# Optimization experiments

Hardware: AMD Instinct MI355X
Metric: run time of the kernel (lower is better)

The kernel has to match this reference:

```python
import jax, jax.numpy as jnp
import numpy as np

N_NODES = 100000
N_EDGES = 1600000
H_IN = 128
H_OUT = 128
ELU_ALPHA = 0.1


def setup_inputs() -> dict:
    key = jax.random.key(0)
    k = jax.random.split(key, 6)
    x = jax.random.normal(k[0], (N_NODES, H_IN), dtype=jnp.float32)
    edge_index = jax.random.randint(k[1], (2, N_EDGES), 0, N_NODES, dtype=jnp.int64)
    s = 1.0 / np.sqrt(H_IN)
    W_conv = jax.random.uniform(k[2], (H_IN, H_OUT), jnp.float32, -s, s)
    b_conv = jnp.zeros((H_OUT,), jnp.float32)
    W_skip = jax.random.uniform(k[3], (H_IN, H_OUT), jnp.float32, -s, s)
    b_skip = jax.random.uniform(k[4], (H_OUT,), jnp.float32, -s, s)
    return {"x": x, "edge_index": edge_index, "W_conv": W_conv,
            "b_conv": b_conv, "W_skip": W_skip, "b_skip": b_skip}


def reference(x, edge_index, W_conv, b_conv, W_skip, b_skip):
    # GCNConv(improved=True): add self-loops with weight 2.0, symmetric norm.
    N = x.shape[0]
    src, dst = edge_index[0], edge_index[1]
    # degree = incoming edge weights (1.0 each) + 2.0 self-loop weight
    deg = jnp.zeros((N,), x.dtype).at[dst].add(1.0) + 2.0
    dinv = jax.lax.rsqrt(deg)                     # deg >= 2 always
    norm = dinv[src] * dinv[dst]                  # [E]
    h = x @ W_conv                                # [N, H_OUT]
    # scatter-add of normalized messages over real edges
    agg = jax.ops.segment_sum(norm[:, None] * h[src], dst, num_segments=N)
    # self-loop contribution: weight 2 * dinv[i]^2
    agg = agg + (2.0 * dinv * dinv)[:, None] * h
    out = agg + b_conv + x @ W_skip + b_skip
    # Dropout(p=0.1) in eval mode = identity; ELU(alpha=0.1)
    return jnp.where(out > 0, out, ELU_ALPHA * (jnp.exp(out) - 1.0))
```

## Files before the change

kernel.cpp:

```cpp
#include <hip/hip_runtime.h>
#include <hip/hip_bf16.h>

#define H 128
#define BW 128
#define BSH 7
#define NB 256

typedef __attribute__((ext_vector_type(8))) short short8;
typedef __attribute__((ext_vector_type(4))) float f32x4;

__device__ inline unsigned short f2bf(float f) {
    union { float f; unsigned int u; } v; v.f = f;
    unsigned int r = (v.u + 0x7fffu + ((v.u >> 16) & 1u)) >> 16;
    return (unsigned short)r;
}
__device__ inline float bf2f(unsigned short h) {
    union { unsigned int u; float f; } v; v.u = ((unsigned int)h) << 16;
    return v.f;
}

__global__ __launch_bounds__(256) void p1_hist(const int* __restrict__ ei,
                                               int* __restrict__ counts,
                                               int E, int nbu, int chunk) {
    __shared__ int h[1024];
    for (int i = threadIdx.x; i < nbu; i += 256) h[i] = 0;
    __syncthreads();
    const int b = blockIdx.x;
    const int lo = b * chunk;
    const int hi = min(E, lo + chunk);
    for (int e = lo + threadIdx.x; e < hi; e += 256)
        atomicAdd(&h[ei[E + e] >> BSH], 1);
    __syncthreads();
    for (int i = threadIdx.x; i < nbu; i += 256) counts[b * nbu + i] = h[i];
}

__global__ __launch_bounds__(NB) void p2_scan(const int* __restrict__ counts,
                                              int* __restrict__ scanned,
                                              int* __restrict__ btot, int nbu) {
    __shared__ int s[NB];
    const int k = blockIdx.x, t = threadIdx.x;
    int v = counts[t * nbu + k];
    s[t] = v;
    __syncthreads();
    for (int off = 1; off < NB; off <<= 1) {
        int a = (t >= off) ? s[t - off] : 0;
        __syncthreads();
        s[t] += a;
        __syncthreads();
    }
    scanned[t * nbu + k] = s[t] - v;
    if (t == NB - 1) btot[k] = s[t];
}

__global__ __launch_bounds__(1024) void p3_scan(const int* __restrict__ btot,
                                                int* __restrict__ cstart,
                                                int nbu, int E) {
    __shared__ int s[1024];
    const int t = threadIdx.x;
    int v = (t < nbu) ? btot[t] : 0;
    s[t] = v;
    __syncthreads();
    for (int off = 1; off < 1024; off <<= 1) {
        int a = (t >= off) ? s[t - off] : 0;
        __syncthreads();
        s[t] += a;
        __syncthreads();
    }
    if (t < nbu) cstart[t] = s[t] - v;
    if (t == 0) cstart[nbu] = E;
}

__global__ __launch_bounds__(256) void p5_scatter(const int* __restrict__ ei,
                                                  const int* __restrict__ cstart,
                                                  const int* __restrict__ scanned,
                                                  int* __restrict__ tmp,
                                                  int E, int nbu, int chunk) {
    __shared__ int lbase[1024];
    const int b = blockIdx.x;
    for (int k = threadIdx.x; k < nbu; k += 256)
        lbase[k] = cstart[k] + scanned[b * nbu + k];
    __syncthreads();
    const int lo = b * chunk;
    const int hi = min(E, lo + chunk);
    for (int e = lo + threadIdx.x; e < hi; e += 256) {
        int s = ei[e], d = ei[E + e];
        int slot = atomicAdd(&lbase[d >> BSH], 1);
        tmp[slot] = ((d & (BW - 1)) << 17) | s;
    }
}

__global__ __launch_bounds__(256) void csr_kernel(const int* __restrict__ tmp,
                                                  const int* __restrict__ cstart,
                                                  const float* __restrict__ invs,
                                                  int* __restrict__ entries,
                                                  int* __restrict__ rstart,
                                                  float* __restrict__ dinv,
                                                  float* __restrict__ ainv,
                                                  int N, int E) {
    __shared__ int ldeg[BW];
    __shared__ int lscan[BW];
    __shared__ int lcur[BW];
    const int b = blockIdx.x;
    const int nstart = b << BSH;
    const int estart = cstart[b];
    const int eend = cstart[b + 1];
    const int t = threadIdx.x;

    if (t < BW) ldeg[t] = 0;
    __syncthreads();
    for (int i = estart + t; i < eend; i += 256)
        atomicAdd(&ldeg[(tmp[i] >> 17) & (BW - 1)], 1);
    __syncthreads();
    if (t < BW) lscan[t] = ldeg[t];
    __syncthreads();
    #pragma unroll
    for (int off = 1; off < BW; off <<= 1) {
        int a = 0;
        if (t < BW && t >= off) a = lscan[t - off];
        __syncthreads();
        if (t < BW) lscan[t] += a;
        __syncthreads();
    }
    if (t < BW) {
        int excl = lscan[t] - ldeg[t];
        lcur[t] = excl;
        int n = nstart + t;
        if (n < N) {
            float dv = rsqrtf((float)ldeg[t] + 2.0f);
            rstart[n] = estart + excl;
            dinv[n] = dv;
            ainv[n] = dv * invs[n];
        }
    }
    __syncthreads();
    for (int i = estart + t; i < eend; i += 256) {
        int v = tmp[i];
        int sl = atomicAdd(&lcur[(v >> 17) & (BW - 1)], 1);
        entries[estart + sl] = v & 0x1FFFF;
    }
    if (b == 0 && t == 0) rstart[N] = E;
}

__global__ __launch_bounds__(256) void quant_kernel(const float* __restrict__ x,
                                                    uint* __restrict__ xq,
                                                    float* __restrict__ invs, int N) {
    int node = blockIdx.x * 8 + (threadIdx.x >> 5);
    if (node >= N) return;
    int l32 = threadIdx.x & 31;
    float4 v = ((const float4*)x)[node * 32 + l32];
    float m = fmaxf(fmaxf(fabsf(v.x), fabsf(v.y)), fmaxf(fabsf(v.z), fabsf(v.w)));
    #pragma unroll
    for (int mk = 1; mk < 32; mk <<= 1) m = fmaxf(m, __shfl_xor(m, mk));
    m = fmaxf(m, 1e-30f);
    float s = 127.0f / m;
    int q0 = min(255, max(0, (int)rintf(v.x * s) + 128));
    int q1 = min(255, max(0, (int)rintf(v.y * s) + 128));
    int q2 = min(255, max(0, (int)rintf(v.z * s) + 128));
    int q3 = min(255, max(0, (int)rintf(v.w * s) + 128));
    xq[node * 32 + l32] = (uint)q0 | ((uint)q1 << 8) | ((uint)q2 << 16) | ((uint)q3 << 24);
    if (l32 == 0) invs[node] = m / 127.0f;
}

__global__ __launch_bounds__(256) void wpack_kernel(const float* __restrict__ Wc,
                                                    const float* __restrict__ Ws,
                                                    short8* __restrict__ wp) {
    int t = blockIdx.x * 256 + threadIdx.x;
    if (t >= 2048) return;
    int lane = t & 63;
    int nt = (t >> 6) & 7;
    int ks = t >> 9;
    int kbase = ks * 32 + (lane >> 4) * 8;
    int col = nt * 16 + (lane & 15);
    short8 whc, whs, wls;
    #pragma unroll
    for (int j = 0; j < 8; ++j) {
        float wc = Wc[(kbase + j) * H + col];
        float ws = Ws[(kbase + j) * H + col];
        unsigned short hc = f2bf(wc);
        unsigned short hs = f2bf(ws);
        whc[j] = (short)hc;
        whs[j] = (short)hs;
        wls[j] = (short)f2bf(ws - bf2f(hs));
    }
    int base = (ks * 8 + nt) * 64 + lane;
    wp[base] = whc;
    wp[2048 + base] = whs;
    wp[4096 + base] = wls;
}

__global__ __launch_bounds__(256) void agg_kernel(const int* __restrict__ entries,
                                                  const int* __restrict__ rstart,
                                                  const float* __restrict__ dinv,
                                                  const float* __restrict__ ainv,
                                                  const float* __restrict__ invs,
                                                  const uint* __restrict__ xq,
                                                  unsigned short* __restrict__ z, int N) {
    int node = blockIdx.x * 4 + (threadIdx.x >> 6);
    if (node >= N) return;
    int lane = threadIdx.x & 63;
    int l16 = lane & 15;
    int q4 = lane >> 4;
    int start = rstart[node];
    int end = rstart[node + 1];
    float dd = dinv[node];
    const uint2* x2 = (const uint2*)xq;
    float acc[8] = {0.f, 0.f, 0.f, 0.f, 0.f, 0.f, 0.f, 0.f};
    float sumw = 0.f;

    for (int c = start; c < end; c += 64) {
        int rem = end - c;
        int src = 0;
        float w = 0.f;
        if (lane < rem) {
            src = entries[c + lane];
            w = ainv[src] * dd;
        }
        int cnt = rem < 64 ? rem : 64;
        int iters = (cnt + 3) >> 2;
        #pragma unroll 4
        for (int t = 0; t < iters; ++t) {
            int idx = 4 * t + q4;
            int ss = __shfl(src, idx);
            float wv = __shfl(w, idx);
            uint2 q = x2[ss * 16 + l16];
            sumw += wv;
            acc[0] += wv * (float)(q.x & 0xffu);
            acc[1] += wv * (float)((q.x >> 8) & 0xffu);
            acc[2] += wv * (float)((q.x >> 16) & 0xffu);
            acc[3] += wv * (float)(q.x >> 24);
            acc[4] += wv * (float)(q.y & 0xffu);
            acc[5] += wv * (float)((q.y >> 8) & 0xffu);
            acc[6] += wv * (float)((q.y >> 16) & 0xffu);
            acc[7] += wv * (float)(q.y >> 24);
        }
    }

    #pragma unroll
    for (int j = 0; j < 8; ++j) {
        acc[j] += __shfl_xor(acc[j], 16);
        acc[j] += __shfl_xor(acc[j], 32);
    }
    sumw += __shfl_xor(sumw, 16);
    sumw += __shfl_xor(sumw, 32);

    if (q4 == 0) {
        float wself = 2.f * dd * dd * invs[node];
        uint2 qs = x2[node * 16 + l16];
        sumw += wself;
        acc[0] += wself * (float)(qs.x & 0xffu);
        acc[1] += wself * (float)((qs.x >> 8) & 0xffu);
        acc[2] += wself * (float)((qs.x >> 16) & 0xffu);
        acc[3] += wself * (float)(qs.x >> 24);
        acc[4] += wself * (float)(qs.y & 0xffu);
        acc[5] += wself * (float)((qs.y >> 8) & 0xffu);
        acc[6] += wself * (float)((qs.y >> 16) & 0xffu);
        acc[7] += wself * (float)(qs.y >> 24);
        float off = 128.f * sumw;
        uint4 o;
        o.x = (uint)f2bf(acc[0] - off) | ((uint)f2bf(acc[1] - off) << 16);
        o.y = (uint)f2bf(acc[2] - off) | ((uint)f2bf(acc[3] - off) << 16);
        o.z = (uint)f2bf(acc[4] - off) | ((uint)f2bf(acc[5] - off) << 16);
        o.w = (uint)f2bf(acc[6] - off) | ((uint)f2bf(acc[7] - off) << 16);
        ((uint4*)z)[node * 16 + l16] = o;
    }
}

__global__ __launch_bounds__(256) void gemm_kernel(const unsigned short* __restrict__ zb,
                                                   const float* __restrict__ x,
                                                   const short8* __restrict__ wp,
                                                   const float* __restrict__ bc,
                                                   const float* __restrict__ bsk,
                                                   float* __restrict__ out, int N) {
    const int lane = threadIdx.x & 63;
    const int wave = threadIdx.x >> 6;
    const int m = lane & 15;
    const int quad = lane >> 4;
    const int row = blockIdx.x * 64 + wave * 16 + m;
    const bool rowok = row < N;

    f32x4 acc[8];
    #pragma unroll
    for (int i = 0; i < 8; ++i) acc[i] = (f32x4){0.f, 0.f, 0.f, 0.f};

    #pragma unroll
    for (int ks = 0; ks < 4; ++ks) {
        const int k0 = ks * 32 + quad * 8;
        short8 za = {0, 0, 0, 0, 0, 0, 0, 0};
        short8 xa_h = {0, 0, 0, 0, 0, 0, 0, 0};
        short8 xa_l = {0, 0, 0, 0, 0, 0, 0, 0};
        if (rowok) {
            za = ((const short8*)zb)[(row * H + k0) >> 3];
            float4 a = *(const float4*)&x[row * H + k0];
            float4 b = *(const float4*)&x[row * H + k0 + 4];
            float xv[8] = {a.x, a.y, a.z, a.w, b.x, b.y, b.z, b.w};
            #pragma unroll
            for (int j = 0; j < 8; ++j) {
                unsigned short h = f2bf(xv[j]);
                xa_h[j] = (short)h;
                xa_l[j] = (short)f2bf(xv[j] - bf2f(h));
            }
        }
        #pragma unroll
        for (int nt = 0; nt < 8; ++nt) {
            int base = (ks * 8 + nt) * 64 + lane;
            short8 bch = wp[base];
            short8 bsh = wp[2048 + base];
            short8 bsl = wp[4096 + base];
            acc[nt] = __builtin_amdgcn_mfma_f32_16x16x32_bf16(za, bch, acc[nt], 0, 0, 0);
            acc[nt] = __builtin_amdgcn_mfma_f32_16x16x32_bf16(xa_h, bsh, acc[nt], 0, 0, 0);
            acc[nt] = __builtin_amdgcn_mfma_f32_16x16x32_bf16(xa_l, bsh, acc[nt], 0, 0, 0);
            acc[nt] = __builtin_amdgcn_mfma_f32_16x16x32_bf16(xa_h, bsl, acc[nt], 0, 0, 0);
        }
    }

    const int orow_base = blockIdx.x * 64 + wave * 16 + quad * 4;
    #pragma unroll
    for (int nt = 0; nt < 8; ++nt) {
        int col = nt * 16 + m;
        float bias = bc[col] + bsk[col];
        #pragma unroll
        for (int r = 0; r < 4; ++r) {
            int orow = orow_base + r;
            if (orow < N) {
                float v = acc[nt][r] + bias;
                v = v > 0.f ? v : 0.1f * (__expf(v) - 1.f);
                out[orow * H + col] = v;
            }
        }
    }
}

extern "C" void kernel_launch(void* const* d_in, const int* in_sizes, int n_in,
                              void* d_out, int out_size, void* d_ws, size_t ws_size,
                              hipStream_t stream) {
    const float* x   = (const float*)d_in[0];
    const int*   ei  = (const int*)d_in[1];
    const float* Wc  = (const float*)d_in[2];
    const float* bc  = (const float*)d_in[3];
    const float* Wsk = (const float*)d_in[4];
    const float* bsk = (const float*)d_in[5];
    float* out = (float*)d_out;

    const int N = in_sizes[0] / H;
    const int E = in_sizes[1] / 2;
    const int nbu = (N + BW - 1) / BW;
    const int chunk = (E + NB - 1) / NB;

    char* w = (char*)d_ws;
    int*            cstart  = (int*)w;
    int*            btot    = (int*)(w + 8192);
    short8*         wp      = (short8*)(w + 16384);
    int*            rstart  = (int*)(w + 131072);
    float*          dinv    = (float*)(w + 589824);
    float*          invs    = (float*)(w + 1048576);
    float*          ainv    = (float*)(w + 1507328);
    int*            counts  = (int*)(w + 2097152);
    int*            scanned = (int*)(w + 3145728);
    int*            entries = (int*)(w + 4194304);
    int*            tmp     = (int*)(w + 11010048);
    unsigned short* z       = (unsigned short*)(w + 11010048);
    uint*           xq      = (uint*)(w + 38535168);

    quant_kernel<<<(N + 7) / 8, 256, 0, stream>>>(x, xq, invs, N);

    p1_hist<<<NB, 256, 0, stream>>>(ei, counts, E, nbu, chunk);
    p2_scan<<<nbu, NB, 0, stream>>>(counts, scanned, btot, nbu);
    p3_scan<<<1, 1024, 0, stream>>>(btot, cstart, nbu, E);
    p5_scatter<<<NB, 256, 0, stream>>>(ei, cstart, scanned, tmp, E, nbu, chunk);
    csr_kernel<<<nbu, 256, 0, stream>>>(tmp, cstart, invs, entries, rstart, dinv, ainv, N, E);

    wpack_kernel<<<8, 256, 0, stream>>>(Wc, Wsk, wp);

    agg_kernel<<<(N + 3) / 4, 256, 0, stream>>>(entries, rstart, dinv, ainv, invs, xq, z, N);

    gemm_kernel<<<(N + 63) / 64, 256, 0, stream>>>(z, x, wp, bc, bsk, out, N);
}
```

Baseline: 269.9 us.

## Precompute fp16 edge weights in CSR build, widen agg loads, fuse small kernels

Splits CSR construction into two passes so the second pass can compute each edge's normalized weight (ainv[src]*dinv[dst]) and store it as fp16 beside the source index. This removes the random ainv gather from the aggregation loop. The aggregation kernel now loads 16-byte rows with 8 lanes per neighbor, so 8 neighbors are processed per iteration instead of 4, and the self-loop weight is precomputed. The single-block p3 scan is folded into p5_scatter and wpack into quant_kernel, cutting launches. The costs are an extra CSR kernel pass, a redundant btot scan in every scatter block, and fp16 rounding of the edge weights.

```diff
diff --git a/kernel.cpp b/kernel.cpp
--- a/kernel.cpp
+++ b/kernel.cpp
@@ -1,5 +1,6 @@
 #include <hip/hip_runtime.h>
 #include <hip/hip_bf16.h>
+#include <hip/hip_fp16.h>
 
 #define H 128
 #define BW 128
@@ -52,54 +53,62 @@
     if (t == NB - 1) btot[k] = s[t];
 }
 
-__global__ __launch_bounds__(1024) void p3_scan(const int* __restrict__ btot,
-                                                int* __restrict__ cstart,
-                                                int nbu, int E) {
-    __shared__ int s[1024];
-    const int t = threadIdx.x;
-    int v = (t < nbu) ? btot[t] : 0;
-    s[t] = v;
-    __syncthreads();
-    for (int off = 1; off < 1024; off <<= 1) {
-        int a = (t >= off) ? s[t - off] : 0;
-        __syncthreads();
-        s[t] += a;
-        __syncthreads();
-    }
-    if (t < nbu) cstart[t] = s[t] - v;
-    if (t == 0) cstart[nbu] = E;
-}
-
 __global__ __launch_bounds__(256) void p5_scatter(const int* __restrict__ ei,
-                                                  const int* __restrict__ cstart,
+                                                  const int* __restrict__ btot,
                                                   const int* __restrict__ scanned,
                                                   int* __restrict__ tmp,
+                                                  int* __restrict__ cstart,
                                                   int E, int nbu, int chunk) {
-    __shared__ int lbase[1024];
+    __shared__ int sc[1024];
+    __shared__ int part[256];
+    __shared__ int lb[1024];
+    const int t = threadIdx.x;
     const int b = blockIdx.x;
-    for (int k = threadIdx.x; k < nbu; k += 256)
-        lbase[k] = cstart[k] + scanned[b * nbu + k];
+    const int base = t * 4;
+    int v0 = (base + 0 < nbu) ? btot[base + 0] : 0;
+    int v1 = (base + 1 < nbu) ? btot[base + 1] : 0;
+    int v2 = (base + 2 < nbu) ? btot[base + 2] : 0;
+    int v3 = (base + 3 < nbu) ? btot[base + 3] : 0;
+    int s1 = v0 + v1, s2 = s1 + v2, s3 = s2 + v3;
+    part[t] = s3;
+    __syncthreads();
+    for (int off = 1; off < 256; off <<= 1) {
+        int a = (t >= off) ? part[t - off] : 0;
+        __syncthreads();
+        part[t] += a;
+        __syncthreads();
+    }
+    int add = (t > 0) ? part[t - 1] : 0;
+    sc[base + 0] = add;
+    sc[base + 1] = add + v0;
+    sc[base + 2] = add + s1;
+    sc[base + 3] = add + s2;
+    __syncthreads();
+    if (b == 0) {
+        for (int k = t; k < nbu; k += 256) cstart[k] = sc[k];
+        if (t == 0) cstart[nbu] = E;
+    }
+    for (int k = t; k < nbu; k += 256) lb[k] = sc[k] + scanned[b * nbu + k];
     __syncthreads();
     const int lo = b * chunk;
     const int hi = min(E, lo + chunk);
-    for (int e = lo + threadIdx.x; e < hi; e += 256) {
+    for (int e = lo + t; e < hi; e += 256) {
         int s = ei[e], d = ei[E + e];
-        int slot = atomicAdd(&lbase[d >> BSH], 1);
+        int slot = atomicAdd(&lb[d >> BSH], 1);
         tmp[slot] = ((d & (BW - 1)) << 17) | s;
     }
 }
 
-__global__ __launch_bounds__(256) void csr_kernel(const int* __restrict__ tmp,
-                                                  const int* __restrict__ cstart,
-                                                  const float* __restrict__ invs,
-                                                  int* __restrict__ entries,
-                                                  int* __restrict__ rstart,
-                                                  float* __restrict__ dinv,
-                                                  float* __restrict__ ainv,
-                                                  int N, int E) {
+__global__ __launch_bounds__(256) void csra_kernel(const int* __restrict__ tmp,
+                                                   const int* __restrict__ cstart,
+                                                   const float* __restrict__ invs,
+                                                   int* __restrict__ rstart,
+                                                   float* __restrict__ dinv,
+                                                   float* __restrict__ ainv,
+                                                   float* __restrict__ selfw,
+                                                   int N, int E) {
     __shared__ int ldeg[BW];
     __shared__ int lscan[BW];
-    __shared__ int lcur[BW];
     const int b = blockIdx.x;
     const int nstart = b << BSH;
     const int estart = cstart[b];
@@ -123,88 +132,119 @@
     }
     if (t < BW) {
         int excl = lscan[t] - ldeg[t];
-        lcur[t] = excl;
         int n = nstart + t;
         if (n < N) {
+            float iv = invs[n];
             float dv = rsqrtf((float)ldeg[t] + 2.0f);
             rstart[n] = estart + excl;
             dinv[n] = dv;
-            ainv[n] = dv * invs[n];
-        }
-    }
-    __syncthreads();
+            ainv[n] = dv * iv;
+            selfw[n] = 2.0f * dv * dv * iv;
+        }
+    }
+    if (b == 0 && t == 0) rstart[N] = E;
+}
+
+__global__ __launch_bounds__(256) void csrb_kernel(const int* __restrict__ tmp,
+                                                   const int* __restrict__ cstart,
+                                                   const int* __restrict__ rstart,
+                                                   const float* __restrict__ dinv,
+                                                   const float* __restrict__ ainv,
+                                                   int* __restrict__ entries,
+                                                   unsigned short* __restrict__ wgt,
+                                                   int N, int E) {
+    __shared__ int lcur[BW];
+    __shared__ float ldv[BW];
+    const int b = blockIdx.x;
+    const int nstart = b << BSH;
+    const int t = threadIdx.x;
+    if (t < BW) {
+        int n = nstart + t;
+        lcur[t] = (n < N) ? rstart[n] : 0;
+        ldv[t] = (n < N) ? dinv[n] : 0.f;
+    }
+    __syncthreads();
+    const int estart = cstart[b];
+    const int eend = cstart[b + 1];
     for (int i = estart + t; i < eend; i += 256) {
         int v = tmp[i];
-        int sl = atomicAdd(&lcur[(v >> 17) & (BW - 1)], 1);
-        entries[estart + sl] = v & 0x1FFFF;
-    }
-    if (b == 0 && t == 0) rstart[N] = E;
+        int ld = (v >> 17) & (BW - 1);
+        int src = v & 0x1FFFF;
+        float w = ainv[src] * ldv[ld];
+        int slot = atomicAdd(&lcur[ld], 1);
+        entries[slot] = src;
+        wgt[slot] = __half_as_ushort(__float2half(w));
+    }
 }
 
 __global__ __launch_bounds__(256) void quant_kernel(const float* __restrict__ x,
+                                                    const float* __restrict__ Wc,
+                                                    const float* __restrict__ Ws,
                                                     uint* __restrict__ xq,
-                                                    float* __restrict__ invs, int N) {
+                                                    float* __restrict__ invs,
+                                                    short8* __restrict__ wp, int N) {
     int node = blockIdx.x * 8 + (threadIdx.x >> 5);
-    if (node >= N) return;
-    int l32 = threadIdx.x & 31;
-    float4 v = ((const float4*)x)[node * 32 + l32];
-    float m = fmaxf(fmaxf(fabsf(v.x), fabsf(v.y)), fmaxf(fabsf(v.z), fabsf(v.w)));
-    #pragma unroll
-    for (int mk = 1; mk < 32; mk <<= 1) m = fmaxf(m, __shfl_xor(m, mk));
-    m = fmaxf(m, 1e-30f);
-    float s = 127.0f / m;
-    int q0 = min(255, max(0, (int)rintf(v.x * s) + 128));
-    int q1 = min(255, max(0, (int)rintf(v.y * s) + 128));
-    int q2 = min(255, max(0, (int)rintf(v.z * s) + 128));
-    int q3 = min(255, max(0, (int)rintf(v.w * s) + 128));
-    xq[node * 32 + l32] = (uint)q0 | ((uint)q1 << 8) | ((uint)q2 << 16) | ((uint)q3 << 24);
-    if (l32 == 0) invs[node] = m / 127.0f;
-}
-
-__global__ __launch_bounds__(256) void wpack_kernel(const float* __restrict__ Wc,
-                                                    const float* __restrict__ Ws,
-                                                    short8* __restrict__ wp) {
-    int t = blockIdx.x * 256 + threadIdx.x;
-    if (t >= 2048) return;
-    int lane = t & 63;
-    int nt = (t >> 6) & 7;
-    int ks = t >> 9;
-    int kbase = ks * 32 + (lane >> 4) * 8;
-    int col = nt * 16 + (lane & 15);
-    short8 whc, whs, wls;
-    #pragma unroll
-    for (int j = 0; j < 8; ++j) {
-        float wc = Wc[(kbase + j) * H + col];
-        float ws = Ws[(kbase + j) * H + col];
-        unsigned short hc = f2bf(wc);
-        unsigned short hs = f2bf(ws);
-        whc[j] = (short)hc;
-        whs[j] = (short)hs;
-        wls[j] = (short)f2bf(ws - bf2f(hs));
-    }
-    int base = (ks * 8 + nt) * 64 + lane;
-    wp[base] = whc;
-    wp[2048 + base] = whs;
-    wp[4096 + base] = wls;
+    if (node < N) {
+        int l32 = threadIdx.x & 31;
+        float4 v = ((const float4*)x)[node * 32 + l32];
+        float m = fmaxf(fmaxf(fabsf(v.x), fabsf(v.y)), fmaxf(fabsf(v.z), fabsf(v.w)));
+        #pragma unroll
+        for (int mk = 1; mk < 32; mk <<= 1) m = fmaxf(m, __shfl_xor(m, mk));
+        m = fmaxf(m, 1e-30f);
+        float s = 127.0f / m;
+        int q0 = min(255, max(0, (int)rintf(v.x * s) + 128));
+        int q1 = min(255, max(0, (int)rintf(v.y * s) + 128));
+        int q2 = min(255, max(0, (int)rintf(v.z * s) + 128));
+        int q3 = min(255, max(0, (int)rintf(v.w * s) + 128));
+        xq[node * 32 + l32] = (uint)q0 | ((uint)q1 << 8) | ((uint)q2 << 16) | ((uint)q3 << 24);
+        if (l32 == 0) invs[node] = m / 127.0f;
+    }
+    if (blockIdx.x < 8) {
+        int t = blockIdx.x * 256 + threadIdx.x;
+        int lane = t & 63;
+        int nt = (t >> 6) & 7;
+        int ks = t >> 9;
+        int kbase = ks * 32 + (lane >> 4) * 8;
+        int col = nt * 16 + (lane & 15);
+        short8 whc, whs, wls;
+        #pragma unroll
+        for (int j = 0; j < 8; ++j) {
+            float wc = Wc[(kbase + j) * H + col];
+            float ws = Ws[(kbase + j) * H + col];
+            unsigned short hc = f2bf(wc);
+            unsigned short hs = f2bf(ws);
+            whc[j] = (short)hc;
+            whs[j] = (short)hs;
+            wls[j] = (short)f2bf(ws - bf2f(hs));
+        }
+        int base = (ks * 8 + nt) * 64 + lane;
+        wp[base] = whc;
+        wp[2048 + base] = whs;
+        wp[4096 + base] = wls;
+    }
 }
 
 __global__ __launch_bounds__(256) void agg_kernel(const int* __restrict__ entries,
+                                                  const unsigned short* __restrict__ wgt,
                                                   const int* __restrict__ rstart,
-                                                  const float* __restrict__ dinv,
-                                                  const float* __restrict__ ainv,
-                                                  const float* __restrict__ invs,
+                                                  const float* __restrict__ selfw,
                                                   const uint* __restrict__ xq,
                                                   unsigned short* __restrict__ z, int N) {
     int node = blockIdx.x * 4 + (threadIdx.x >> 6);
     if (node >= N) return;
-    int lane = threadIdx.x & 63;
-    int l16 = lane & 15;
-    int q4 = lane >> 4;
+    const int lane = threadIdx.x & 63;
+    const int l8 = lane & 7;
+    const int g = lane >> 3;
+    const uint4* x4 = (const uint4*)xq;
+
     int start = rstart[node];
     int end = rstart[node + 1];
-    float dd = dinv[node];
-    const uint2* x2 = (const uint2*)xq;
-    float acc[8] = {0.f, 0.f, 0.f, 0.f, 0.f, 0.f, 0.f, 0.f};
+    float sw = selfw[node];
+    uint4 qs = x4[node * 8 + l8];
+
+    float acc[16];
+    #pragma unroll
+    for (int j = 0; j < 16; ++j) acc[j] = 0.f;
     float sumw = 0.f;
 
     for (int c = start; c < end; c += 64) {
@@ -213,55 +253,69 @@
         float w = 0.f;
         if (lane < rem) {
             src = entries[c + lane];
-            w = ainv[src] * dd;
+            w = __half2float(__ushort_as_half(wgt[c + lane]));
         }
         int cnt = rem < 64 ? rem : 64;
-        int iters = (cnt + 3) >> 2;
+        int iters = (cnt + 7) >> 3;
         #pragma unroll 4
         for (int t = 0; t < iters; ++t) {
-            int idx = 4 * t + q4;
+            int idx = 8 * t + g;
             int ss = __shfl(src, idx);
             float wv = __shfl(w, idx);
-            uint2 q = x2[ss * 16 + l16];
+            uint4 q = x4[ss * 8 + l8];
             sumw += wv;
-            acc[0] += wv * (float)(q.x & 0xffu);
-            acc[1] += wv * (float)((q.x >> 8) & 0xffu);
-            acc[2] += wv * (float)((q.x >> 16) & 0xffu);
-            acc[3] += wv * (float)(q.x >> 24);
-            acc[4] += wv * (float)(q.y & 0xffu);
-            acc[5] += wv * (float)((q.y >> 8) & 0xffu);
-            acc[6] += wv * (float)((q.y >> 16) & 0xffu);
-            acc[7] += wv * (float)(q.y >> 24);
-        }
-    }
-
+            acc[0]  += wv * (float)(q.x & 0xffu);
+            acc[1]  += wv * (float)((q.x >> 8) & 0xffu);
+            acc[2]  += wv * (float)((q.x >> 16) & 0xffu);
+            acc[3]  += wv * (float)(q.x >> 24);
+            acc[4]  += wv * (float)(q.y & 0xffu);
+            acc[5]  += wv * (float)((q.y >> 8) & 0xffu);
+            acc[6]  += wv * (float)((q.y >> 16) & 0xffu);
+            acc[7]  += wv * (float)(q.y >> 24);
+            acc[8]  += wv * (float)(q.z & 0xffu);
+            acc[9]  += wv * (float)((q.z >> 8) & 0xffu);
+            acc[10] += wv * (float)((q.z >> 16) & 0xffu);
+            acc[11] += wv * (float)(q.z >> 24);
+            acc[12] += wv * (float)(q.w & 0xffu);
+            acc[13] += wv * (float)((q.w >> 8) & 0xffu);
+            acc[14] += wv * (float)((q.w >> 16) & 0xffu);
+            acc[15] += wv * (float)(q.w >> 24);
+        }
+    }
+
+    #pragma unroll
+    for (int j = 0; j < 16; ++j) acc[j] += __shfl_xor(acc[j], 8);
+    const int hi = g & 1;
+    float r[8];
+    #pragma unroll
+    for (int j = 0; j < 8; ++j) r[j] = hi ? acc[j + 8] : acc[j];
     #pragma unroll
     for (int j = 0; j < 8; ++j) {
-        acc[j] += __shfl_xor(acc[j], 16);
-        acc[j] += __shfl_xor(acc[j], 32);
-    }
+        r[j] += __shfl_xor(r[j], 16);
+        r[j] += __shfl_xor(r[j], 32);
+    }
+    sumw += __shfl_xor(sumw, 8);
     sumw += __shfl_xor(sumw, 16);
     sumw += __shfl_xor(sumw, 32);
 
-    if (q4 == 0) {
-        float wself = 2.f * dd * dd * invs[node];
-        uint2 qs = x2[node * 16 + l16];
-        sumw += wself;
-        acc[0] += wself * (float)(qs.x & 0xffu);
-        acc[1] += wself * (float)((qs.x >> 8) & 0xffu);
-        acc[2] += wself * (float)((qs.x >> 16) & 0xffu);
-        acc[3] += wself * (float)(qs.x >> 24);
-        acc[4] += wself * (float)(qs.y & 0xffu);
-        acc[5] += wself * (float)((qs.y >> 8) & 0xffu);
-        acc[6] += wself * (float)((qs.y >> 16) & 0xffu);
-        acc[7] += wself * (float)(qs.y >> 24);
-        float off = 128.f * sumw;
+    if (lane < 16) {
+        uint qa = hi ? qs.z : qs.x;
+        uint qb = hi ? qs.w : qs.y;
+        r[0] += sw * (float)(qa & 0xffu);
+        r[1] += sw * (float)((qa >> 8) & 0xffu);
+        r[2] += sw * (float)((qa >> 16) & 0xffu);
+        r[3] += sw * (float)(qa >> 24);
+        r[4] += sw * (float)(qb & 0xffu);
+        r[5] += sw * (float)((qb >> 8) & 0xffu);
+        r[6] += sw * (float)((qb >> 16) & 0xffu);
+        r[7] += sw * (float)(qb >> 24);
+        float off = 128.f * (sumw + sw);
         uint4 o;
-        o.x = (uint)f2bf(acc[0] - off) | ((uint)f2bf(acc[1] - off) << 16);
-        o.y = (uint)f2bf(acc[2] - off) | ((uint)f2bf(acc[3] - off) << 16);
-        o.z = (uint)f2bf(acc[4] - off) | ((uint)f2bf(acc[5] - off) << 16);
-        o.w = (uint)f2bf(acc[6] - off) | ((uint)f2bf(acc[7] - off) << 16);
-        ((uint4*)z)[node * 16 + l16] = o;
+        o.x = (uint)f2bf(r[0] - off) | ((uint)f2bf(r[1] - off) << 16);
+        o.y = (uint)f2bf(r[2] - off) | ((uint)f2bf(r[3] - off) << 16);
+        o.z = (uint)f2bf(r[4] - off) | ((uint)f2bf(r[5] - off) << 16);
+        o.w = (uint)f2bf(r[6] - off) | ((uint)f2bf(r[7] - off) << 16);
+        ((uint4*)z)[node * 16 + 2 * l8 + (lane >> 3)] = o;
     }
 }
 
@@ -347,31 +401,31 @@
     const int chunk = (E + NB - 1) / NB;
 
     char* w = (char*)d_ws;
-    int*            cstart  = (int*)w;
-    int*            btot    = (int*)(w + 8192);
-    short8*         wp      = (short8*)(w + 16384);
+    short8*         wp      = (short8*)w;
     int*            rstart  = (int*)(w + 131072);
-    float*          dinv    = (float*)(w + 589824);
-    float*          invs    = (float*)(w + 1048576);
-    float*          ainv    = (float*)(w + 1507328);
-    int*            counts  = (int*)(w + 2097152);
-    int*            scanned = (int*)(w + 3145728);
-    int*            entries = (int*)(w + 4194304);
-    int*            tmp     = (int*)(w + 11010048);
-    unsigned short* z       = (unsigned short*)(w + 11010048);
-    uint*           xq      = (uint*)(w + 38535168);
-
-    quant_kernel<<<(N + 7) / 8, 256, 0, stream>>>(x, xq, invs, N);
+    float*          selfw   = (float*)(w + 589824);
+    int*            entries = (int*)(w + 1048576);
+    unsigned short* wgt     = (unsigned short*)(w + 7471104);
+    uint*           xq      = (uint*)(w + 10747904);
+    unsigned short* z       = (unsigned short*)(w + 23592960);
+    float*          invs    = (float*)(w + 23592960);
+    float*          dinv    = (float*)(w + 23992960);
+    float*          ainv    = (float*)(w + 24392960);
+    int*            cstart  = (int*)(w + 24792960);
+    int*            btot    = (int*)(w + 24796160);
+    int*            counts  = (int*)(w + 24799360);
+    int*            scanned = (int*)(w + 25600128);
+    int*            tmp     = (int*)(w + 26400896);
+
+    quant_kernel<<<(N + 7) / 8, 256, 0, stream>>>(x, Wc, Wsk, xq, invs, wp, N);
 
     p1_hist<<<NB, 256, 0, stream>>>(ei, counts, E, nbu, chunk);
     p2_scan<<<nbu, NB, 0, stream>>>(counts, scanned, btot, nbu);
-    p3_scan<<<1, 1024, 0, stream>>>(btot, cstart, nbu, E);
-    p5_scatter<<<NB, 256, 0, stream>>>(ei, cstart, scanned, tmp, E, nbu, chunk);
-    csr_kernel<<<nbu, 256, 0, stream>>>(tmp, cstart, invs, entries, rstart, dinv, ainv, N, E);
-
-    wpack_kernel<<<8, 256, 0, stream>>>(Wc, Wsk, wp);
-
-    agg_kernel<<<(N + 3) / 4, 256, 0, stream>>>(entries, rstart, dinv, ainv, invs, xq, z, N);
+    p5_scatter<<<NB, 256, 0, stream>>>(ei, btot, scanned, tmp, cstart, E, nbu, chunk);
+    csra_kernel<<<nbu, 256, 0, stream>>>(tmp, cstart, invs, rstart, dinv, ainv, selfw, N, E);
+    csrb_kernel<<<nbu, 256, 0, stream>>>(tmp, cstart, rstart, dinv, ainv, entries, wgt, N, E);
+
+    agg_kernel<<<(N + 3) / 4, 256, 0, stream>>>(entries, wgt, rstart, selfw, xq, z, N);
 
     gemm_kernel<<<(N + 63) / 64, 256, 0, stream>>>(z, x, wp, bc, bsk, out, N);
 }
```

Result: slower. 336.1 us (+24.5%).
